# Kernel tuning notes

Measured on AMD Instinct MI355X. Metric: run time of the kernel, lower is better.

Reference implementation:

```python
import jax, jax.numpy as jnp
import numpy as np

N_NODES = 20000
N_EDGES = 320000
HIDDEN = 512
EDGE_DIM = 64
LN_EPS = 1e-5


def mish(x):
    return x * jnp.tanh(jax.nn.softplus(x))


def setup_inputs() -> dict:
    key = jax.random.key(0)
    ks = jax.random.split(key, 8)
    s = lambda fan_in: 1.0 / np.sqrt(fan_in)
    return {
        "x": jax.random.normal(ks[0], (N_NODES, HIDDEN), dtype=jnp.float32),
        "edge_index": jax.random.randint(ks[1], (2, N_EDGES), 0, N_NODES, dtype=jnp.int64),
        "edge_attr": jax.random.normal(ks[2], (N_EDGES, EDGE_DIM), dtype=jnp.float32),
        "W1": jax.random.normal(ks[3], (2 * HIDDEN + EDGE_DIM, HIDDEN), dtype=jnp.float32) * s(2 * HIDDEN + EDGE_DIM),
        "b1": jnp.zeros((HIDDEN,), dtype=jnp.float32),
        "W2": jax.random.normal(ks[4], (HIDDEN, HIDDEN), dtype=jnp.float32) * s(HIDDEN),
        "b2": jnp.zeros((HIDDEN,), dtype=jnp.float32),
        "W3": jax.random.normal(ks[5], (2 * HIDDEN, HIDDEN), dtype=jnp.float32) * s(2 * HIDDEN),
        "b3": jnp.zeros((HIDDEN,), dtype=jnp.float32),
        "W4": jax.random.normal(ks[6], (HIDDEN, HIDDEN), dtype=jnp.float32) * s(HIDDEN),
        "b4": jnp.zeros((HIDDEN,), dtype=jnp.float32),
        "gamma": jnp.ones((HIDDEN,), dtype=jnp.float32),
        "beta": jnp.zeros((HIDDEN,), dtype=jnp.float32),
    }


def reference(x, edge_index, edge_attr, W1, b1, W2, b2, W3, b3, W4, b4, gamma, beta):
    src, dst = edge_index[0], edge_index[1]
    # msg_mlp: Linear -> Mish -> Linear -> Mish on [E, 2H+Edim]
    edge_feat = jnp.concatenate([x[src], x[dst], edge_attr], axis=-1)  # [E, 2H+Edim]
    h = mish(edge_feat @ W1 + b1)
    messages = mish(h @ W2 + b2)  # [E, H]
    # scatter-add messages to destination nodes
    agg = jax.ops.segment_sum(messages, dst, num_segments=x.shape[0])  # [N, H]
    # update_mlp: Linear -> Mish -> Linear
    u = mish(jnp.concatenate([x, agg], axis=-1) @ W3 + b3)
    out = u @ W4 + b4  # [N, H]
    # residual + LayerNorm
    y = x + out
    mu = jnp.mean(y, axis=-1, keepdims=True)
    var = jnp.mean(jnp.square(y - mu), axis=-1, keepdims=True)
    return (y - mu) * jax.lax.rsqrt(var + LN_EPS) * gamma + beta
```

## Files before the change

### kernel.cpp

```cpp
#include <hip/hip_runtime.h>
#include <cstdint>
#include <cstddef>

#define NNODES 20000
#define NEDGES 320000
#define HID 512
#define EDIM 64
#define KFEAT (2*HID + EDIM)

typedef __bf16 bf16x8 __attribute__((ext_vector_type(8)));
typedef short short8 __attribute__((ext_vector_type(8)));
typedef float f32x4 __attribute__((ext_vector_type(4)));

#define AM_NODE 1
#define AM_DIR  2
#define EP_BF16    0
#define EP_F32     2
#define EP_BF16L   3

__device__ __forceinline__ uint16_t f2bf(float f){
  uint32_t u = __float_as_uint(f);
  u += 0x7FFFu + ((u >> 16) & 1u);
  return (uint16_t)(u >> 16);
}
__device__ __forceinline__ float bf2f(uint16_t h){
  return __uint_as_float((uint32_t)h << 16);
}
__device__ __forceinline__ float mishf(float v){
  float e = __expf(fminf(v, 18.f));
  float n = e * (e + 2.f);
  return v * __fdividef(n, n + 2.f);
}
__device__ __forceinline__ void gl_lds16(const void* g, void* l){
  __builtin_amdgcn_global_load_lds(
      (const __attribute__((address_space(1))) uint32_t*)g,
      (__attribute__((address_space(3))) uint32_t*)l, 16, 0, 0);
}

__global__ void detect_idx(const int* __restrict__ e, int* __restrict__ flag){
  int i = blockIdx.x * 256 + threadIdx.x;
  if (e[2*i + 1] != 0) atomicOr(flag, 1);
}
__global__ void norm_idx(const int* __restrict__ e, const int* __restrict__ flag,
                         int* __restrict__ s, int* __restrict__ d){
  int i = blockIdx.x * 256 + threadIdx.x;
  if (i >= NEDGES) return;
  int sv, dv;
  if (*flag){ sv = e[i];     dv = e[NEDGES + i]; }
  else      { sv = e[2*i];   dv = e[2*NEDGES + 2*i]; }
  sv = sv < 0 ? 0 : (sv > NNODES-1 ? NNODES-1 : sv);
  dv = dv < 0 ? 0 : (dv > NNODES-1 ? NNODES-1 : dv);
  s[i] = sv; d[i] = dv;
}

__global__ void hist_k(const int* __restrict__ d, int* __restrict__ cnt){
  int i = blockIdx.x * 256 + threadIdx.x;
  if (i < NEDGES) atomicAdd(&cnt[d[i]], 1);
}
__global__ __launch_bounds__(256)
void scan_k(const int* __restrict__ cnt, int* __restrict__ rp, int* __restrict__ cur){
  const int SEG = (NNODES + 255) / 256;
  const int t = threadIdx.x;
  const int lo = t * SEG;
  const int hi = (lo + SEG < NNODES) ? lo + SEG : NNODES;
  int s = 0;
  for (int i = lo; i < hi; ++i) s += cnt[i];
  __shared__ int sh[256];
  sh[t] = s; __syncthreads();
  for (int o = 1; o < 256; o <<= 1){
    int v = (t >= o) ? sh[t - o] : 0;
    __syncthreads();
    sh[t] += v;
    __syncthreads();
  }
  int pre = t ? sh[t-1] : 0;
  for (int i = lo; i < hi; ++i){
    rp[i] = pre; cur[i] = pre; pre += cnt[i];
  }
  if (t == 255) rp[NNODES] = sh[255];
}
__global__ void permute_k(const int* __restrict__ srcN, const int* __restrict__ dstN,
                          int* __restrict__ cur, int* __restrict__ srcS,
                          int* __restrict__ eidx){
  int i = blockIdx.x * 256 + threadIdx.x;
  if (i < NEDGES){
    int d = dstN[i];
    int p = atomicAdd(&cur[d], 1);
    srcS[p] = srcN[i];
    eidx[p] = i;
  }
}
__global__ void fill_dstS(const int* __restrict__ rp, int* __restrict__ dstS){
  int n = blockIdx.x;
  int lo = rp[n], hi = rp[n+1];
  for (int e = lo + threadIdx.x; e < hi; e += 64) dstS[e] = n;
}

__global__ void cast_bf16_vec(const float4* __restrict__ in, ushort4* __restrict__ out, int n4){
  int i = blockIdx.x * 256 + threadIdx.x;
  if (i < n4){
    float4 v = in[i];
    ushort4 o; o.x = f2bf(v.x); o.y = f2bf(v.y); o.z = f2bf(v.z); o.w = f2bf(v.w);
    out[i] = o;
  }
}
__global__ void transpose_cast(const float* __restrict__ W, uint16_t* __restrict__ WT, int K, int N){
  int k = blockIdx.x * 256 + threadIdx.x;
  int n = blockIdx.y;
  if (k < K) WT[(size_t)n * K + k] = f2bf(W[(size_t)k * N + n]);
}

template<int AMODE, int EPI, int KTOT, int BPQ>
__global__ __launch_bounds__(256, 2)
void gemm_k(const uint16_t* __restrict__ A0, const uint16_t* __restrict__ A1,
            const uint16_t* __restrict__ BT, const float* __restrict__ bias,
            uint16_t* __restrict__ Cb, float* __restrict__ Cf,
            int bstr, int cstr, int m0base, int M, int crowOff)
{
  __shared__ __align__(16) char smem[32768];
  char* As = smem;
  char* Bs = smem + 16384;
  const int t = threadIdx.x;
  const int m0 = m0base + blockIdx.y * 128;
  const int n0 = blockIdx.x * 128;
  const int srow = t >> 3;
  const int c8   = t & 7;
  const int scol = ((c8 ^ (srow & 7)) << 3);
  const int ldst = srow * 128 + c8 * 16;

  const uint16_t* as0[4]; const uint16_t* as1[4];
  #pragma unroll
  for (int i = 0; i < 4; ++i){
    int gm = m0 + srow + 32*i;
    if (gm > M - 1) gm = M - 1;
    if (AMODE == AM_NODE){
      as0[i] = A0 + (size_t)gm * HID;
      as1[i] = A1 + (size_t)gm * HID;
    } else {
      as0[i] = A0 + (size_t)gm * KTOT;
      as1[i] = A0;
    }
  }
  const uint16_t* brow[4];
  #pragma unroll
  for (int i = 0; i < 4; ++i){
    int nr = n0 + srow + 32*i;
    if (BPQ) brow[i] = BT + (size_t)(nr & (HID-1))*bstr + (nr >> 9)*HID;
    else     brow[i] = BT + (size_t)nr*bstr;
  }

  const int lane = t & 63;
  const int wv = t >> 6;
  const int wm = (wv >> 1) * 64;
  const int wn = (wv & 1) * 64;
  const int l15 = lane & 15;
  const int lk16 = (lane >> 4) << 4;
  const int swz = (l15 & 7) << 4;

  f32x4 acc[4][4] = {};

  const int NK = KTOT / 64;
  for (int kk = 0; kk < NK; ++kk){
    const int k0 = kk * 64;
    #pragma unroll
    for (int i = 0; i < 4; ++i){
      const uint16_t* g;
      if (AMODE == AM_NODE){
        g = (k0 < HID) ? as0[i] + (k0 + scol) : as1[i] + (k0 - HID + scol);
      } else {
        g = as0[i] + (k0 + scol);
      }
      gl_lds16(g, As + i*4096 + ldst);
    }
    #pragma unroll
    for (int i = 0; i < 4; ++i)
      gl_lds16(brow[i] + (k0 + scol), Bs + i*4096 + ldst);
    __syncthreads();
    #pragma unroll
    for (int ks = 0; ks < 2; ++ks){
      bf16x8 af[4], bfr[4];
      #pragma unroll
      for (int i = 0; i < 4; ++i){
        const int ar = wm + i*16 + l15;
        af[i] = *(const bf16x8*)(As + ar*128 + ((ks*64 + lk16) ^ swz));
      }
      #pragma unroll
      for (int j = 0; j < 4; ++j){
        const int br = wn + j*16 + l15;
        bfr[j] = *(const bf16x8*)(Bs + br*128 + ((ks*64 + lk16) ^ swz));
      }
      #pragma unroll
      for (int i = 0; i < 4; ++i)
        #pragma unroll
        for (int j = 0; j < 4; ++j)
          acc[i][j] = __builtin_amdgcn_mfma_f32_16x16x32_bf16(af[i], bfr[j], acc[i][j], 0, 0, 0);
    }
    __syncthreads();
  }

  #pragma unroll
  for (int i = 0; i < 4; ++i){
    const int rb = wm + i*16 + ((lane >> 4) << 2);
    #pragma unroll
    for (int j = 0; j < 4; ++j){
      const int gcol = n0 + wn + j*16 + l15;
      const float bv = (EPI == EP_BF16L) ? 0.f : bias[gcol];
      #pragma unroll
      for (int r = 0; r < 4; ++r){
        const int grow = m0 + rb + r;
        if (grow < M){
          float v = acc[i][j][r] + bv;
          if (EPI == EP_BF16){
            Cb[(size_t)(grow - crowOff) * cstr + gcol] = f2bf(mishf(v));
          } else if (EPI == EP_BF16L){
            Cb[(size_t)(grow - crowOff) * cstr + gcol] = f2bf(v);
          } else {
            Cf[(size_t)grow * cstr + gcol] = v;
          }
        }
      }
    }
  }
}

__global__ __launch_bounds__(256, 4)
void eh_k(const uint16_t* __restrict__ eab, const uint16_t* __restrict__ PQb,
          const int* __restrict__ idx,
          const uint16_t* __restrict__ w1t, const float* __restrict__ b1,
          uint16_t* __restrict__ hb, int m0base, int crowOff)
{
  __shared__ __align__(16) char smem[32768];
  const int t = threadIdx.x;
  const int m0 = m0base + blockIdx.x * 32;
  const int lane = t & 63;
  const int wv = t >> 6;
  const int l15 = lane & 15;
  const int lg = lane >> 4;
  const int* srcS = idx;
  const int* dstS = idx + NEDGES;
  const int* eidx = idx + 2*NEDGES;

  int eidxr[2];
  #pragma unroll
  for (int fr = 0; fr < 2; ++fr) eidxr[fr] = eidx[m0 + fr*16 + l15];

  f32x4 acc[2][8] = {};

  #pragma unroll
  for (int ks = 0; ks < 2; ++ks){
    bf16x8 bF[8];
    #pragma unroll
    for (int fc = 0; fc < 8; ++fc){
      int n = wv*128 + fc*16 + l15;
      bF[fc] = *(const bf16x8*)(w1t + (size_t)n*KFEAT + 2*HID + ks*32 + lg*8);
    }
    #pragma unroll
    for (int fr = 0; fr < 2; ++fr){
      bf16x8 av = *(const bf16x8*)(eab + (size_t)eidxr[fr]*EDIM + ks*32 + lg*8);
      #pragma unroll
      for (int fc = 0; fc < 8; ++fc)
        acc[fr][fc] = __builtin_amdgcn_mfma_f32_16x16x32_bf16(av, bF[fc], acc[fr][fc], 0, 0, 0);
    }
  }

  char* slab = smem + wv*8192;
  const float4 b1v0 = *(const float4*)(b1 + wv*128 + l15*4);
  const float4 b1v1 = *(const float4*)(b1 + wv*128 + 64 + l15*4);
  #pragma unroll
  for (int fr = 0; fr < 2; ++fr){
    #pragma unroll
    for (int fc = 0; fc < 8; ++fc){
      #pragma unroll
      for (int r = 0; r < 4; ++r){
        int row = lg*4 + r;
        int cb = ((fc*16 + l15)*4) ^ ((lg & 1) << 6);
        *(float*)(slab + row*512 + cb) = acc[fr][fc][r];
      }
    }
    asm volatile("s_waitcnt lgkmcnt(0)" ::: "memory");
    __builtin_amdgcn_sched_barrier(0);
    #pragma unroll
    for (int i = 0; i < 4; ++i){
      int row = i*4 + lg;
      int grow = m0 + fr*16 + row;
      int s = srcS[grow];
      int d = dstS[grow];
      float4 v0 = *(const float4*)(slab + row*512 + ((l15*16) ^ ((i & 1) << 6)));
      float4 v1 = *(const float4*)(slab + row*512 + ((256 + l15*16) ^ ((i & 1) << 6)));
      ushort4 p0 = *(const ushort4*)(PQb + (size_t)s*1024 + wv*128 + l15*4);
      ushort4 p1 = *(const ushort4*)(PQb + (size_t)s*1024 + wv*128 + 64 + l15*4);
      ushort4 q0 = *(const ushort4*)(PQb + (size_t)d*1024 + 512 + wv*128 + l15*4);
      ushort4 q1 = *(const ushort4*)(PQb + (size_t)d*1024 + 512 + wv*128 + 64 + l15*4);
      ushort4 h0, h1;
      h0.x = f2bf(mishf(v0.x + bf2f(p0.x) + bf2f(q0.x) + b1v0.x));
      h0.y = f2bf(mishf(v0.y + bf2f(p0.y) + bf2f(q0.y) + b1v0.y));
      h0.z = f2bf(mishf(v0.z + bf2f(p0.z) + bf2f(q0.z) + b1v0.z));
      h0.w = f2bf(mishf(v0.w + bf2f(p0.w) + bf2f(q0.w) + b1v0.w));
      h1.x = f2bf(mishf(v1.x + bf2f(p1.x) + bf2f(q1.x) + b1v1.x));
      h1.y = f2bf(mishf(v1.y + bf2f(p1.y) + bf2f(q1.y) + b1v1.y));
      h1.z = f2bf(mishf(v1.z + bf2f(p1.z) + bf2f(q1.z) + b1v1.z));
      h1.w = f2bf(mishf(v1.w + bf2f(p1.w) + bf2f(q1.w) + b1v1.w));
      size_t hrow = (size_t)(grow - crowOff) * HID + wv*128;
      *(ushort4*)(hb + hrow + l15*4) = h0;
      *(ushort4*)(hb + hrow + 64 + l15*4) = h1;
    }
    asm volatile("s_waitcnt lgkmcnt(0)" ::: "memory");
    __builtin_amdgcn_sched_barrier(0);
  }
}

__global__ __launch_bounds__(128)
void gather_agg(const uint16_t* __restrict__ msg, const int* __restrict__ rp,
                float* __restrict__ agg, int e0, int e1){
  const int n = blockIdx.x;
  int lo = rp[n], hi = rp[n+1];
  if (lo < e0) lo = e0;
  if (hi > e1) hi = e1;
  if (lo >= hi) return;
  const int t = threadIdx.x;
  float4 a = {0.f, 0.f, 0.f, 0.f};
  for (int e = lo; e < hi; ++e){
    ushort4 m = ((const ushort4*)(msg + (size_t)(e - e0) * HID))[t];
    a.x += bf2f(m.x); a.y += bf2f(m.y); a.z += bf2f(m.z); a.w += bf2f(m.w);
  }
  float4* ap = ((float4*)(agg + (size_t)n * HID)) + t;
  float4 c = *ap;
  c.x += a.x; c.y += a.y; c.z += a.z; c.w += a.w;
  *ap = c;
}

__global__ __launch_bounds__(128)
void resid_ln(const float* __restrict__ x, const float* __restrict__ ob,
              const float* __restrict__ gamma, const float* __restrict__ beta,
              float* __restrict__ y){
  const int row = blockIdx.x;
  const int t = threadIdx.x;
  const float4 xv = ((const float4*)(x + (size_t)row * HID))[t];
  const float4 ov = ((const float4*)(ob + (size_t)row * HID))[t];
  float4 s4;
  s4.x = xv.x + ov.x; s4.y = xv.y + ov.y; s4.z = xv.z + ov.z; s4.w = xv.w + ov.w;
  float s = s4.x + s4.y + s4.z + s4.w;
  float q = s4.x*s4.x + s4.y*s4.y + s4.z*s4.z + s4.w*s4.w;
  #pragma unroll
  for (int o = 32; o; o >>= 1){
    s += __shfl_xor(s, o, 64);
    q += __shfl_xor(q, o, 64);
  }
  __shared__ float ss[2], qq[2];
  if ((t & 63) == 0){ ss[t >> 6] = s; qq[t >> 6] = q; }
  __syncthreads();
  const float S = ss[0] + ss[1], Q = qq[0] + qq[1];
  const float mu = S * (1.0f / HID);
  const float var = Q * (1.0f / HID) - mu * mu;
  const float inv = rsqrtf(var + 1e-5f);
  const float4 g = ((const float4*)gamma)[t];
  const float4 b = ((const float4*)beta)[t];
  float4 o;
  o.x = (s4.x - mu) * inv * g.x + b.x;
  o.y = (s4.y - mu) * inv * g.y + b.y;
  o.z = (s4.z - mu) * inv * g.z + b.z;
  o.w = (s4.w - mu) * inv * g.w + b.w;
  ((float4*)(y + (size_t)row * HID))[t] = o;
}

extern "C" void kernel_launch(void* const* d_in, const int* in_sizes, int n_in,
                              void* d_out, int out_size, void* d_ws, size_t ws_size,
                              hipStream_t stream)
{
  const float* x    = (const float*)d_in[0];
  const int*   ei   = (const int*)d_in[1];
  const float* ea   = (const float*)d_in[2];
  const float* W1   = (const float*)d_in[3];
  const float* b1   = (const float*)d_in[4];
  const float* W2   = (const float*)d_in[5];
  const float* b2   = (const float*)d_in[6];
  const float* W3   = (const float*)d_in[7];
  const float* b3   = (const float*)d_in[8];
  const float* W4   = (const float*)d_in[9];
  const float* b4   = (const float*)d_in[10];
  const float* gmm  = (const float*)d_in[11];
  const float* bet  = (const float*)d_in[12];
  float* out = (float*)d_out;

  uint8_t* w = (uint8_t*)d_ws;
  size_t off = 0;
  auto alloc = [&](size_t bytes) -> void* {
    void* p = w + off;
    off += (bytes + 255) & ~(size_t)255;
    return p;
  };
  uint16_t* xb   = (uint16_t*)alloc((size_t)NNODES*HID*2);
  uint16_t* w1t  = (uint16_t*)alloc((size_t)HID*KFEAT*2);
  uint16_t* w2t  = (uint16_t*)alloc((size_t)HID*HID*2);
  uint16_t* w3t  = (uint16_t*)alloc((size_t)HID*1024*2);
  uint16_t* w4t  = (uint16_t*)alloc((size_t)HID*HID*2);
  uint16_t* PQb  = (uint16_t*)alloc((size_t)NNODES*1024*2);
  float*    agg  = (float*)alloc((size_t)NNODES*HID*4);
  uint16_t* aggb = (uint16_t*)alloc((size_t)NNODES*HID*2);
  uint16_t* ub   = (uint16_t*)alloc((size_t)NNODES*HID*2);
  float*    outf = (float*)alloc((size_t)NNODES*HID*4);
  int*      srcN = (int*)alloc((size_t)NEDGES*4);
  int*      dstN = (int*)alloc((size_t)NEDGES*4);
  int*      idxS = (int*)alloc((size_t)NEDGES*4*3);
  int*      cnt  = (int*)alloc((size_t)NNODES*4);
  int*      rp   = (int*)alloc((size_t)(NNODES+1)*4);
  int*      cur  = (int*)alloc((size_t)NNODES*4);
  int*      flag = (int*)alloc(256);
  int*      srcS = idxS;
  int*      dstS = idxS + NEDGES;
  int*      eidx = idxS + 2*NEDGES;

  uint16_t* eab = (uint16_t*)outf;

  size_t remain = (ws_size > off) ? ws_size - off : 0;
  size_t maxChunk = remain / ((size_t)HID*2*2);
  long long chunkE = (long long)(maxChunk & ~(size_t)127);
  if (chunkE > NEDGES) chunkE = NEDGES;
  if (chunkE < 128) chunkE = 128;
  uint16_t* hb   = (uint16_t*)alloc((size_t)chunkE*HID*2);
  uint16_t* msgb = (uint16_t*)alloc((size_t)chunkE*HID*2);

  hipMemsetAsync(agg, 0, (size_t)NNODES*HID*4, stream);
  hipMemsetAsync(cnt, 0, (size_t)NNODES*4, stream);
  hipMemsetAsync(flag, 0, 4, stream);

  detect_idx<<<64, 256, 0, stream>>>(ei, flag);
  norm_idx<<<(NEDGES+255)/256, 256, 0, stream>>>(ei, flag, srcN, dstN);
  hist_k<<<(NEDGES+255)/256, 256, 0, stream>>>(dstN, cnt);
  scan_k<<<1, 256, 0, stream>>>(cnt, rp, cur);
  permute_k<<<(NEDGES+255)/256, 256, 0, stream>>>(srcN, dstN, cur, srcS, eidx);
  fill_dstS<<<NNODES, 64, 0, stream>>>(rp, dstS);

  cast_bf16_vec<<<(NNODES*HID/4+255)/256, 256, 0, stream>>>((const float4*)x, (ushort4*)xb, NNODES*HID/4);
  cast_bf16_vec<<<(NEDGES*EDIM/4+255)/256, 256, 0, stream>>>((const float4*)ea, (ushort4*)eab, NEDGES*EDIM/4);

  transpose_cast<<<dim3((KFEAT+255)/256, HID), 256, 0, stream>>>(W1, w1t, KFEAT, HID);
  transpose_cast<<<dim3((HID+255)/256,   HID), 256, 0, stream>>>(W2, w2t, HID, HID);
  transpose_cast<<<dim3((1024+255)/256,  HID), 256, 0, stream>>>(W3, w3t, 1024, HID);
  transpose_cast<<<dim3((HID+255)/256,   HID), 256, 0, stream>>>(W4, w4t, HID, HID);

  dim3 gpq(1024/128, (NNODES+127)/128);
  gemm_k<AM_DIR, EP_BF16L, HID, 1><<<gpq, 256, 0, stream>>>(
      xb, nullptr, w1t, b1, PQb, nullptr, KFEAT, 1024, 0, NNODES, 0);

  for (long long e0 = 0; e0 < NEDGES; e0 += chunkE){
    int ce = (int)((NEDGES - e0 < chunkE) ? (NEDGES - e0) : chunkE);
    eh_k<<<(ce+31)/32, 256, 0, stream>>>(eab, PQb, idxS, w1t, b1, hb, (int)e0, (int)e0);
    dim3 g2(HID/128, (ce+127)/128);
    gemm_k<AM_DIR, EP_BF16, HID, 0><<<g2, 256, 0, stream>>>(
        hb, nullptr, w2t, b2, msgb, nullptr, HID, HID, 0, ce, 0);
    gather_agg<<<NNODES, 128, 0, stream>>>(msgb, rp, agg, (int)e0, (int)(e0+ce));
  }

  cast_bf16_vec<<<(NNODES*HID/4+255)/256, 256, 0, stream>>>((const float4*)agg, (ushort4*)aggb, NNODES*HID/4);

  dim3 g3(HID/128, (NNODES+127)/128);
  gemm_k<AM_NODE, EP_BF16, 1024, 0><<<g3, 256, 0, stream>>>(
      xb, aggb, w3t, b3, ub, nullptr, 1024, HID, 0, NNODES, 0);
  gemm_k<AM_DIR, EP_F32, HID, 0><<<g3, 256, 0, stream>>>(
      ub, nullptr, w4t, b4, nullptr, outf, HID, HID, 0, NNODES, 0);

  resid_ln<<<NNODES, 128, 0, stream>>>(x, outf, gmm, bet, out);
}
```

Baseline: 938.8 us.

## Remap GEMM blocks per XCD and move W2 bias+Mish into gather

Adds an XCD-aware block swizzle to the GEMM so each of the 8 chiplets handles a contiguous band of row tiles, meant to improve L2 reuse of the A rows. Grid heights are padded to 160 tiles and edge chunks rounded to 1024 so the remap condition holds. The bias add and Mish after the second edge GEMM are moved out of that GEMM's epilogue and into the gather-aggregation loop. Mish costs the same either way since each edge is gathered once, but the GEMM epilogue gets lighter. Padded rows rely on the existing M clamp and bounds guards, and the extra padded tiles do redundant work.

```diff
diff --git a/kernel.cpp b/kernel.cpp
--- a/kernel.cpp
+++ b/kernel.cpp
@@ -17,6 +17,7 @@
 #define EP_BF16    0
 #define EP_F32     2
 #define EP_BF16L   3
+#define EP_RAW     5
 
 __device__ __forceinline__ uint16_t f2bf(float f){
   uint32_t u = __float_as_uint(f);
@@ -121,8 +122,17 @@
   char* As = smem;
   char* Bs = smem + 16384;
   const int t = threadIdx.x;
-  const int m0 = m0base + blockIdx.y * 128;
-  const int n0 = blockIdx.x * 128;
+  const int ntx = gridDim.x, nty = gridDim.y;
+  int bx = blockIdx.x, by = blockIdx.y;
+  if ((nty & 7) == 0){
+    int flat = by * ntx + bx;
+    int xcd = flat & 7;
+    int i = flat >> 3;
+    by = xcd * (nty >> 3) + i / ntx;
+    bx = i % ntx;
+  }
+  const int m0 = m0base + by * 128;
+  const int n0 = bx * 128;
   const int srow = t >> 3;
   const int c8   = t & 7;
   const int scol = ((c8 ^ (srow & 7)) << 3);
@@ -204,7 +214,7 @@
     #pragma unroll
     for (int j = 0; j < 4; ++j){
       const int gcol = n0 + wn + j*16 + l15;
-      const float bv = (EPI == EP_BF16L) ? 0.f : bias[gcol];
+      const float bv = (EPI == EP_BF16L || EPI == EP_RAW) ? 0.f : bias[gcol];
       #pragma unroll
       for (int r = 0; r < 4; ++r){
         const int grow = m0 + rb + r;
@@ -212,7 +222,7 @@
           float v = acc[i][j][r] + bv;
           if (EPI == EP_BF16){
             Cb[(size_t)(grow - crowOff) * cstr + gcol] = f2bf(mishf(v));
-          } else if (EPI == EP_BF16L){
+          } else if (EPI == EP_BF16L || EPI == EP_RAW){
             Cb[(size_t)(grow - crowOff) * cstr + gcol] = f2bf(v);
           } else {
             Cf[(size_t)grow * cstr + gcol] = v;
@@ -311,17 +321,22 @@
 
 __global__ __launch_bounds__(128)
 void gather_agg(const uint16_t* __restrict__ msg, const int* __restrict__ rp,
-                float* __restrict__ agg, int e0, int e1){
+                const float* __restrict__ b2, float* __restrict__ agg,
+                int e0, int e1){
   const int n = blockIdx.x;
   int lo = rp[n], hi = rp[n+1];
   if (lo < e0) lo = e0;
   if (hi > e1) hi = e1;
   if (lo >= hi) return;
   const int t = threadIdx.x;
+  const float4 bv = ((const float4*)b2)[t];
   float4 a = {0.f, 0.f, 0.f, 0.f};
   for (int e = lo; e < hi; ++e){
     ushort4 m = ((const ushort4*)(msg + (size_t)(e - e0) * HID))[t];
-    a.x += bf2f(m.x); a.y += bf2f(m.y); a.z += bf2f(m.z); a.w += bf2f(m.w);
+    a.x += mishf(bf2f(m.x) + bv.x);
+    a.y += mishf(bf2f(m.y) + bv.y);
+    a.z += mishf(bf2f(m.z) + bv.z);
+    a.w += mishf(bf2f(m.w) + bv.w);
   }
   float4* ap = ((float4*)(agg + (size_t)n * HID)) + t;
   float4 c = *ap;
@@ -414,9 +429,9 @@
 
   size_t remain = (ws_size > off) ? ws_size - off : 0;
   size_t maxChunk = remain / ((size_t)HID*2*2);
-  long long chunkE = (long long)(maxChunk & ~(size_t)127);
+  long long chunkE = (long long)(maxChunk & ~(size_t)1023);
   if (chunkE > NEDGES) chunkE = NEDGES;
-  if (chunkE < 128) chunkE = 128;
+  if (chunkE < 1024) chunkE = 1024;
   uint16_t* hb   = (uint16_t*)alloc((size_t)chunkE*HID*2);
   uint16_t* msgb = (uint16_t*)alloc((size_t)chunkE*HID*2);
 
@@ -439,7 +454,7 @@
   transpose_cast<<<dim3((1024+255)/256,  HID), 256, 0, stream>>>(W3, w3t, 1024, HID);
   transpose_cast<<<dim3((HID+255)/256,   HID), 256, 0, stream>>>(W4, w4t, HID, HID);
 
-  dim3 gpq(1024/128, (NNODES+127)/128);
+  dim3 gpq(1024/128, 160);
   gemm_k<AM_DIR, EP_BF16L, HID, 1><<<gpq, 256, 0, stream>>>(
       xb, nullptr, w1t, b1, PQb, nullptr, KFEAT, 1024, 0, NNODES, 0);
 
@@ -447,14 +462,14 @@
     int ce = (int)((NEDGES - e0 < chunkE) ? (NEDGES - e0) : chunkE);
     eh_k<<<(ce+31)/32, 256, 0, stream>>>(eab, PQb, idxS, w1t, b1, hb, (int)e0, (int)e0);
     dim3 g2(HID/128, (ce+127)/128);
-    gemm_k<AM_DIR, EP_BF16, HID, 0><<<g2, 256, 0, stream>>>(
+    gemm_k<AM_DIR, EP_RAW, HID, 0><<<g2, 256, 0, stream>>>(
         hb, nullptr, w2t, b2, msgb, nullptr, HID, HID, 0, ce, 0);
-    gather_agg<<<NNODES, 128, 0, stream>>>(msgb, rp, agg, (int)e0, (int)(e0+ce));
+    gather_agg<<<NNODES, 128, 0, stream>>>(msgb, rp, b2, agg, (int)e0, (int)(e0+ce));
   }
 
   cast_bf16_vec<<<(NNODES*HID/4+255)/256, 256, 0, stream>>>((const float4*)agg, (ushort4*)aggb, NNODES*HID/4);
 
-  dim3 g3(HID/128, (NNODES+127)/128);
+  dim3 g3(HID/128, 160);
   gemm_k<AM_NODE, EP_BF16, 1024, 0><<<g3, 256, 0, stream>>>(
       xb, aggb, w3t, b3, ub, nullptr, 1024, HID, 0, NNODES, 0);
   gemm_k<AM_DIR, EP_F32, HID, 0><<<g3, 256, 0, stream>>>(
```

Result: faster. 912.9 us (-2.8%).
